# Kernel tuning notes

Measured on AMD Instinct MI355X. Metric: run time of the kernel, lower is better.

## Reference

```python
import jax, jax.numpy as jnp
import numpy as np

N_HEADS = 16
ROPE_BASE = 10000.0


def _rotate_half(x):
    d = x.shape[-1] // 2
    return jnp.concatenate([-x[..., d:], x[..., :d]], axis=-1)


def _rope_tables(L, head_dim, dtype):
    inv_freq = 1.0 / (ROPE_BASE ** (jnp.arange(0, head_dim, 2, dtype=jnp.float32) / head_dim))
    t = jnp.arange(L, dtype=jnp.float32)
    freqs = jnp.outer(t, inv_freq)  # [L, head_dim//2]
    # torch code repeats cos/sin along last dim (tile x2) -> concat([c, c])
    cos = jnp.concatenate([jnp.cos(freqs), jnp.cos(freqs)], axis=-1).astype(dtype)
    sin = jnp.concatenate([jnp.sin(freqs), jnp.sin(freqs)], axis=-1).astype(dtype)
    return cos[None, None], sin[None, None]  # [1,1,L,head_dim]


def setup_inputs() -> dict:
    key = jax.random.key(0)
    kx, kq, kk, kv, ko = jax.random.split(key, 5)
    B, L, D = 4, 2048, 1024
    s = 0.02
    return {
        "x": jax.random.normal(kx, (B, L, D), dtype=jnp.float32),
        "Wq": jax.random.normal(kq, (D, D), dtype=jnp.float32) * s,
        "Wk": jax.random.normal(kk, (D, D), dtype=jnp.float32) * s,
        "Wv": jax.random.normal(kv, (D, D), dtype=jnp.float32) * s,
        "Wo": jax.random.normal(ko, (D, D), dtype=jnp.float32) * s,
    }


def reference(x, Wq, Wk, Wv, Wo):
    B, L, D = x.shape
    H = N_HEADS
    hd = D // H

    def split_heads(y):
        return y.reshape(B, L, H, hd).transpose(0, 2, 1, 3)  # [B,H,L,hd]

    q = split_heads(x @ Wq.T)
    k = split_heads(x @ Wk.T)
    v = split_heads(x @ Wv.T)

    cos, sin = _rope_tables(L, hd, x.dtype)
    q = q * cos + _rotate_half(q) * sin
    k = k * cos + _rotate_half(k) * sin

    scale = 1.0 / jnp.sqrt(jnp.asarray(hd, dtype=x.dtype))
    scores = jnp.einsum("bhqd,bhkd->bhqk", q, k) * scale
    attn = jax.nn.softmax(scores, axis=-1)
    out = jnp.einsum("bhqk,bhkd->bhqd", attn, v)
    out = out.transpose(0, 2, 1, 3).reshape(B, L, D)
    return out @ Wo.T
```

## Files before the change

### kernel.cpp

```cpp
#include <hip/hip_runtime.h>


typedef __bf16 bf16_t;
typedef __bf16 bf16x8 __attribute__((ext_vector_type(8)));
typedef __bf16 bf16x4 __attribute__((ext_vector_type(4)));
typedef float  floatx4 __attribute__((ext_vector_type(4)));
typedef unsigned int u32x2 __attribute__((ext_vector_type(2)));

#define B_  4
#define L_  2048
#define D_  1024
#define H_  16
#define HD_ 64
#define M_  (B_*L_)

__device__ __forceinline__ void async_copy16(const bf16_t* g, bf16_t* l) {
  __builtin_amdgcn_global_load_lds(
      (const __attribute__((address_space(1))) void*)g,
      (__attribute__((address_space(3))) void*)l, 16, 0, 0);
}

__device__ __forceinline__ unsigned int pack_bf16(float a, float b) {
  unsigned short ua = __builtin_bit_cast(unsigned short, (bf16_t)a);
  unsigned short ub = __builtin_bit_cast(unsigned short, (bf16_t)b);
  return (unsigned int)ua | ((unsigned int)ub << 16);
}

__device__ __forceinline__ unsigned int cvt_pk(float lo, float hi) {
  unsigned int r;
  asm("v_cvt_pk_bf16_f32 %0, %1, %2" : "=v"(r) : "v"(lo), "v"(hi));
  return r;
}

__global__ void prep_kernel(const float* __restrict__ x,
                            const float* __restrict__ wq, const float* __restrict__ wk,
                            const float* __restrict__ wv, const float* __restrict__ wo,
                            bf16_t* __restrict__ xb,
                            bf16_t* __restrict__ wqb, bf16_t* __restrict__ wkb,
                            bf16_t* __restrict__ wvb, bf16_t* __restrict__ wob,
                            float* __restrict__ cosT, float* __restrict__ sinT)
{
  const int NX = M_*D_;
  const int NW = D_*D_;
  int i = blockIdx.x*256 + threadIdx.x;
  if (i < NX) { xb[i] = (bf16_t)x[i]; return; }
  i -= NX;
  if (i < NW) { wqb[i] = (bf16_t)wq[i]; return; }
  i -= NW;
  if (i < NW) { wkb[i] = (bf16_t)wk[i]; return; }
  i -= NW;
  if (i < NW) { wvb[i] = (bf16_t)wv[i]; return; }
  i -= NW;
  if (i < NW) { wob[i] = (bf16_t)wo[i]; return; }
  i -= NW;
  if (i < L_*32) {
    int f = i >> 11, l = i & 2047;
    double inv = pow(10000.0, -(double)f / 32.0);
    double ang = (double)l * inv;
    cosT[i] = (float)cos(ang);
    sinT[i] = (float)sin(ang);
  }
}

template<int MODE>
__global__ __launch_bounds__(256) void gemm_kernel(
    const bf16_t* __restrict__ A,
    const bf16_t* __restrict__ W0, const bf16_t* __restrict__ W1, const bf16_t* __restrict__ W2,
    bf16_t* __restrict__ C0, bf16_t* __restrict__ C1, bf16_t* __restrict__ C2,
    float* __restrict__ Cf,
    const float* __restrict__ cosT, const float* __restrict__ sinT)
{
  __shared__ __align__(16) bf16_t Sh[16384];
  bf16_t* As = Sh;
  bf16_t* Bs = Sh + 8192;
  const int KD = 1024, ND = 1024;
  int z = (MODE==0) ? (int)blockIdx.z : 0;
  const bf16_t* W = (MODE==1) ? W0 : (z==0 ? W0 : (z==1 ? W1 : W2));
  int m0 = blockIdx.x*128, n0 = blockIdx.y*128;
  int tid = threadIdx.x;
  int wave = tid>>6, lane = tid&63, quad = lane>>4, lr = lane&15;
  int wm = wave>>1, wn = wave&1;
  int srow = lane>>3, sslot = lane&7;

  floatx4 zero4 = {0.f,0.f,0.f,0.f};
  floatx4 acc[4][4];
  #pragma unroll
  for (int i=0;i<4;i++)
    #pragma unroll
    for (int j=0;j<4;j++) acc[i][j] = zero4;

  #pragma unroll 1
  for (int k0 = 0; k0 < KD; k0 += 64) {
    #pragma unroll
    for (int j=0;j<4;j++) {
      int chunk = wave + j*4;
      int row = chunk*8 + srow;
      int col = ((sslot ^ (row&7)) << 3);
      async_copy16(A + (size_t)(m0+row)*KD + k0 + col, &As[chunk*512]);
      async_copy16(W + (size_t)(n0+row)*KD + k0 + col, &Bs[chunk*512]);
    }
    __syncthreads();
    #pragma unroll
    for (int ks=0; ks<2; ks++) {
      bf16x8 af[4], bfr[4];
      #pragma unroll
      for (int mi=0;mi<4;mi++)
        af[mi] = *(const bf16x8*)&As[(wm*64+mi*16+lr)*64 + (((ks*4+quad) ^ (lr&7))<<3)];
      #pragma unroll
      for (int ni=0;ni<4;ni++)
        bfr[ni] = *(const bf16x8*)&Bs[(wn*64+ni*16+lr)*64 + (((ks*4+quad) ^ (lr&7))<<3)];
      #pragma unroll
      for (int mi=0;mi<4;mi++)
        #pragma unroll
        for (int ni=0;ni<4;ni++)
          acc[mi][ni] = __builtin_amdgcn_mfma_f32_16x16x32_bf16(af[mi], bfr[ni], acc[mi][ni], 0,0,0);
    }
    __syncthreads();
  }

  if (MODE==1) {
    #pragma unroll
    for (int mi=0;mi<4;mi++) {
      int row = m0 + wm*64 + mi*16 + quad*4;
      #pragma unroll
      for (int ni=0;ni<4;ni++) {
        int col = n0 + wn*64 + ni*16 + lr;
        #pragma unroll
        for (int r=0;r<4;r++)
          Cf[(size_t)(row+r)*ND + col] = acc[mi][ni][r];
      }
    }
  } else if (z < 2) {
    bf16_t* Cb = (z==0) ? C0 : C1;
    const float sc = (z==0) ? 0.18033688011112042f : 1.0f;
    #pragma unroll
    for (int mi=0;mi<4;mi++) {
      int row = m0 + wm*64 + mi*16 + quad*4;
      int l = row & 2047;
      #pragma unroll
      for (int ni=0;ni<2;ni++) {
        int col = n0 + wn*64 + ni*16 + lr;
        int f = ni*16 + lr;
        float4 cv = *(const float4*)&cosT[f*2048 + l];
        float4 sv = *(const float4*)&sinT[f*2048 + l];
        #pragma unroll
        for (int r=0;r<4;r++) {
          float c = (&cv.x)[r];
          float s = (&sv.x)[r];
          float lo = acc[mi][ni][r], hi = acc[mi][ni+2][r];
          Cb[(size_t)(row+r)*ND + col]      = (bf16_t)((lo*c - hi*s)*sc);
          Cb[(size_t)(row+r)*ND + col + 32] = (bf16_t)((hi*c + lo*s)*sc);
        }
      }
    }
  } else {
    #pragma unroll
    for (int mi=0;mi<4;mi++) {
      int rowm = wm*64 + mi*16 + quad*4;
      #pragma unroll
      for (int ni=0;ni<4;ni++) {
        int coln = wn*64 + ni*16 + lr;
        uint2 val;
        val.x = pack_bf16(acc[mi][ni][0], acc[mi][ni][1]);
        val.y = pack_bf16(acc[mi][ni][2], acc[mi][ni][3]);
        *(uint2*)&Sh[coln*128 + (rowm ^ ((coln&15)<<3))] = val;
      }
    }
    __syncthreads();
    int bb = m0 >> 11, l0 = m0 & 2047;
    #pragma unroll
    for (int rep=0; rep<8; rep++) {
      int idx = rep*256 + tid;
      int coln = idx >> 4, seg = idx & 15;
      bf16x8 v = *(const bf16x8*)&Sh[coln*128 + ((seg*8) ^ ((coln&15)<<3))];
      int cg = n0 + coln;
      *(bf16x8*)&C2[((size_t)((bb<<4) + (cg>>6))*64 + (cg&63))*2048 + l0 + seg*8] = v;
    }
  }
}

__global__ __launch_bounds__(256) void attn_kernel(
    const bf16_t* __restrict__ Q, const bf16_t* __restrict__ K,
    const bf16_t* __restrict__ Vt, bf16_t* __restrict__ O)
{
  __shared__ __align__(16) bf16_t Ks[3][4096];
  __shared__ __align__(16) bf16_t Vs[3][4096];
  int tid = threadIdx.x;
  int wave = tid>>6, lane = tid&63, quad = lane>>4, lr = lane&15;
  int bh = blockIdx.x; int b = bh>>4, h = bh&15;
  int q0 = blockIdx.y*128 + wave*32;
  size_t rowQ = (size_t)b*L_ + q0;

  int slr = (lr&3) | ((lr&4)<<1) | ((lr&8)>>1);
  int srow8 = lane>>3;
  int sslot = lane&7;

  bf16x8 qf[2][2];
  #pragma unroll
  for (int n=0;n<2;n++)
    #pragma unroll
    for (int ks=0;ks<2;ks++)
      qf[n][ks] = *(const bf16x8*)&Q[(rowQ + n*16 + lr)*D_ + h*HD_ + ks*32 + quad*8];

  const bf16_t* Kg = K + (size_t)b*L_*D_ + h*HD_;
  const bf16_t* Vg = Vt + (size_t)bh*HD_*L_;

  bf16x8 onesf;
  #pragma unroll
  for (int j=0;j<8;j++) onesf[j] = (bf16_t)1.0f;

  floatx4 zero4 = {0.f,0.f,0.f,0.f};
  floatx4 accO[2][4];
  floatx4 accS[2];
  accS[0] = zero4; accS[1] = zero4;
  #pragma unroll
  for (int n=0;n<2;n++)
    #pragma unroll
    for (int dt=0;dt<4;dt++) accO[n][dt] = zero4;

  auto stage = [&](int it, int c) {
    #pragma unroll
    for (int j=0;j<2;j++) {
      int row = wave*16 + j*8 + srow8;
      int col = ((sslot ^ (row&7)) << 3);
      async_copy16(Kg + (size_t)(it*64 + row)*D_ + col, &Ks[c][(wave*16 + j*8)*64]);
      async_copy16(Vg + (size_t)row*L_ + it*64 + col,   &Vs[c][(wave*16 + j*8)*64]);
    }
  };

  stage(0, 0);
  stage(1, 1);
  asm volatile("s_waitcnt vmcnt(4)" ::: "memory");
  __builtin_amdgcn_s_barrier();

#define ATTN_BODY(IT, CC, DO_STAGE)                                           \
  {                                                                           \
    if (DO_STAGE) stage((IT)+2, ((CC)+2)%3);                                  \
    floatx4 St[2][4];                                                         \
    _Pragma("unroll")                                                         \
    for (int t=0;t<4;t++) { St[0][t]=zero4; St[1][t]=zero4; }                 \
    _Pragma("unroll")                                                         \
    for (int t=0;t<4;t++) {                                                   \
      _Pragma("unroll")                                                       \
      for (int ks=0;ks<2;ks++) {                                              \
        bf16x8 kf = *(const bf16x8*)&Ks[CC][(t*16+slr)*64 + (((ks*4+quad) ^ (slr&7))<<3)]; \
        St[0][t] = __builtin_amdgcn_mfma_f32_16x16x32_bf16(kf, qf[0][ks], St[0][t], 0,0,0); \
        St[1][t] = __builtin_amdgcn_mfma_f32_16x16x32_bf16(kf, qf[1][ks], St[1][t], 0,0,0); \
      }                                                                       \
    }                                                                         \
    bf16x8 pfv[2][2];                                                         \
    _Pragma("unroll")                                                         \
    for (int n=0;n<2;n++) {                                                   \
      _Pragma("unroll")                                                       \
      for (int hh=0;hh<2;hh++) {                                              \
        unsigned int w00 = cvt_pk(exp2f(St[n][2*hh][0]),   exp2f(St[n][2*hh][1]));   \
        unsigned int w01 = cvt_pk(exp2f(St[n][2*hh][2]),   exp2f(St[n][2*hh][3]));   \
        unsigned int w10 = cvt_pk(exp2f(St[n][2*hh+1][0]), exp2f(St[n][2*hh+1][1])); \
        unsigned int w11 = cvt_pk(exp2f(St[n][2*hh+1][2]), exp2f(St[n][2*hh+1][3])); \
        u32x2 r0 = __builtin_amdgcn_permlane32_swap(w00, w10, false, false);  \
        u32x2 r1 = __builtin_amdgcn_permlane32_swap(w01, w11, false, false);  \
        union { unsigned int u[4]; bf16x8 v; } pu;                            \
        pu.u[0] = r0.x; pu.u[1] = r1.x; pu.u[2] = r0.y; pu.u[3] = r1.y;       \
        pfv[n][hh] = pu.v;                                                    \
      }                                                                       \
    }                                                                         \
    _Pragma("unroll")                                                         \
    for (int dt=0;dt<4;dt++) {                                                \
      _Pragma("unroll")                                                       \
      for (int hh=0;hh<2;hh++) {                                              \
        bf16x8 vf = *(const bf16x8*)&Vs[CC][(dt*16+lr)*64 + (((hh*4+quad) ^ (lr&7))<<3)]; \
        accO[0][dt] = __builtin_amdgcn_mfma_f32_16x16x32_bf16(vf, pfv[0][hh], accO[0][dt], 0,0,0); \
        accO[1][dt] = __builtin_amdgcn_mfma_f32_16x16x32_bf16(vf, pfv[1][hh], accO[1][dt], 0,0,0); \
      }                                                                       \
    }                                                                         \
    accS[0] = __builtin_amdgcn_mfma_f32_16x16x32_bf16(onesf, pfv[0][0], accS[0], 0,0,0); \
    accS[1] = __builtin_amdgcn_mfma_f32_16x16x32_bf16(onesf, pfv[1][0], accS[1], 0,0,0); \
    accS[0] = __builtin_amdgcn_mfma_f32_16x16x32_bf16(onesf, pfv[0][1], accS[0], 0,0,0); \
    accS[1] = __builtin_amdgcn_mfma_f32_16x16x32_bf16(onesf, pfv[1][1], accS[1], 0,0,0); \
    if (DO_STAGE) { asm volatile("s_waitcnt vmcnt(4)" ::: "memory"); }        \
    else          { asm volatile("s_waitcnt vmcnt(0)" ::: "memory"); }        \
    __builtin_amdgcn_s_barrier();                                             \
  }

  #pragma unroll 1
  for (int itb = 0; itb < 30; itb += 3) {
    ATTN_BODY(itb+0, 0, true);
    ATTN_BODY(itb+1, 1, true);
    ATTN_BODY(itb+2, 2, true);
  }
  ATTN_BODY(30, 0, false);
  ATTN_BODY(31, 1, false);
#undef ATTN_BODY

  float inv0 = 1.0f / accS[0][0];
  float inv1 = 1.0f / accS[1][0];
  #pragma unroll
  for (int n=0;n<2;n++) {
    float inv = n ? inv1 : inv0;
    #pragma unroll
    for (int dt=0;dt<4;dt++) {
      uint2 w;
      w.x = cvt_pk(accO[n][dt][0]*inv, accO[n][dt][1]*inv);
      w.y = cvt_pk(accO[n][dt][2]*inv, accO[n][dt][3]*inv);
      *(uint2*)&O[(rowQ + n*16 + lr)*D_ + h*HD_ + dt*16 + quad*4] = w;
    }
  }
}

extern "C" void kernel_launch(void* const* d_in, const int* in_sizes, int n_in,
                              void* d_out, int out_size, void* d_ws, size_t ws_size,
                              hipStream_t stream) {
  const float* x  = (const float*)d_in[0];
  const float* wq = (const float*)d_in[1];
  const float* wk = (const float*)d_in[2];
  const float* wv = (const float*)d_in[3];
  const float* wo = (const float*)d_in[4];

  char* ws = (char*)d_ws;
  bf16_t* xb  = (bf16_t*)(ws);
  bf16_t* Qb  = (bf16_t*)(ws + (size_t)(16u<<20));
  bf16_t* Kb  = (bf16_t*)(ws + (size_t)(32u<<20));
  bf16_t* Vtb = (bf16_t*)(ws + (size_t)(48u<<20));
  bf16_t* wqb = (bf16_t*)(ws + (size_t)(64u<<20));
  bf16_t* wkb = (bf16_t*)(ws + (size_t)(66u<<20));
  bf16_t* wvb = (bf16_t*)(ws + (size_t)(68u<<20));
  bf16_t* wob = (bf16_t*)(ws + (size_t)(70u<<20));
  float* cosT = (float*)(ws + (size_t)(72u<<20));
  float* sinT = (float*)(ws + (size_t)(72u<<20) + (256u<<10));
  bf16_t* Ob = xb;

  prep_kernel<<<49408, 256, 0, stream>>>(x, wq, wk, wv, wo, xb, wqb, wkb, wvb, wob, cosT, sinT);
  gemm_kernel<0><<<dim3(64,8,3), 256, 0, stream>>>(xb, wqb, wkb, wvb, Qb, Kb, Vtb, nullptr, cosT, sinT);
  attn_kernel<<<dim3(64,16), 256, 0, stream>>>(Qb, Kb, Vtb, Ob);
  gemm_kernel<1><<<dim3(64,8,1), 256, 0, stream>>>(Ob, wob, nullptr, nullptr,
                                                   nullptr, nullptr, nullptr, (float*)d_out, cosT, sinT);
}
```

Measured before the change: 302.8 us.

## Vectorize fp32-to-bf16 prep and software-pipeline QK^T one tile ahead in attention

The prep kernel now converts eight floats per thread using float4 loads and a bf16x8 store, which cuts the grid size and the number of memory instructions. The attention loop now double-buffers the score accumulators. It computes the next tile's QK^T MFMAs between the current tile's exp/pack step and its PV MFMAs, so softmax ALU work can overlap matrix work. The wait before each barrier becomes vmcnt(0), which may expose more load latency. The extra score registers raise register pressure and could reduce occupancy.

```diff
diff --git a/kernel.cpp b/kernel.cpp
--- a/kernel.cpp
+++ b/kernel.cpp
@@ -40,19 +40,28 @@
                             bf16_t* __restrict__ wvb, bf16_t* __restrict__ wob,
                             float* __restrict__ cosT, float* __restrict__ sinT)
 {
-  const int NX = M_*D_;
-  const int NW = D_*D_;
+  const int NXv = (M_*D_) >> 3;
+  const int NWv = (D_*D_) >> 3;
+  const int NC  = NXv + 4*NWv;
   int i = blockIdx.x*256 + threadIdx.x;
-  if (i < NX) { xb[i] = (bf16_t)x[i]; return; }
-  i -= NX;
-  if (i < NW) { wqb[i] = (bf16_t)wq[i]; return; }
-  i -= NW;
-  if (i < NW) { wkb[i] = (bf16_t)wk[i]; return; }
-  i -= NW;
-  if (i < NW) { wvb[i] = (bf16_t)wv[i]; return; }
-  i -= NW;
-  if (i < NW) { wob[i] = (bf16_t)wo[i]; return; }
-  i -= NW;
+  if (i < NC) {
+    const float* s; bf16_t* d; size_t o;
+    if (i < NXv) { s = x; d = xb; o = (size_t)i << 3; }
+    else {
+      int r = i - NXv; int w = r >> 17;
+      o = (size_t)(r & (NWv-1)) << 3;
+      s = (w==0)?wq:(w==1)?wk:(w==2)?wv:wo;
+      d = (w==0)?wqb:(w==1)?wkb:(w==2)?wvb:wob;
+    }
+    float4 a = *(const float4*)(s+o);
+    float4 b = *(const float4*)(s+o+4);
+    bf16x8 v;
+    v[0]=(bf16_t)a.x; v[1]=(bf16_t)a.y; v[2]=(bf16_t)a.z; v[3]=(bf16_t)a.w;
+    v[4]=(bf16_t)b.x; v[5]=(bf16_t)b.y; v[6]=(bf16_t)b.z; v[7]=(bf16_t)b.w;
+    *(bf16x8*)(d+o) = v;
+    return;
+  }
+  i -= NC;
   if (i < L_*32) {
     int f = i >> 11, l = i & 2047;
     double inv = pow(10000.0, -(double)f / 32.0);
@@ -218,6 +227,8 @@
     #pragma unroll
     for (int dt=0;dt<4;dt++) accO[n][dt] = zero4;
 
+  floatx4 StA[2][4], StB[2][4];
+
   auto stage = [&](int it, int c) {
     #pragma unroll
     for (int j=0;j<2;j++) {
@@ -230,33 +241,36 @@
 
   stage(0, 0);
   stage(1, 1);
-  asm volatile("s_waitcnt vmcnt(4)" ::: "memory");
+  asm volatile("s_waitcnt vmcnt(0)" ::: "memory");
   __builtin_amdgcn_s_barrier();
 
-#define ATTN_BODY(IT, CC, DO_STAGE)                                           \
-  {                                                                           \
-    if (DO_STAGE) stage((IT)+2, ((CC)+2)%3);                                  \
-    floatx4 St[2][4];                                                         \
+#define QKT_M(CN, SN)                                                         \
     _Pragma("unroll")                                                         \
-    for (int t=0;t<4;t++) { St[0][t]=zero4; St[1][t]=zero4; }                 \
+    for (int t=0;t<4;t++) { SN[0][t]=zero4; SN[1][t]=zero4; }                 \
     _Pragma("unroll")                                                         \
     for (int t=0;t<4;t++) {                                                   \
       _Pragma("unroll")                                                       \
       for (int ks=0;ks<2;ks++) {                                              \
-        bf16x8 kf = *(const bf16x8*)&Ks[CC][(t*16+slr)*64 + (((ks*4+quad) ^ (slr&7))<<3)]; \
-        St[0][t] = __builtin_amdgcn_mfma_f32_16x16x32_bf16(kf, qf[0][ks], St[0][t], 0,0,0); \
-        St[1][t] = __builtin_amdgcn_mfma_f32_16x16x32_bf16(kf, qf[1][ks], St[1][t], 0,0,0); \
+        bf16x8 kf = *(const bf16x8*)&Ks[CN][(t*16+slr)*64 + (((ks*4+quad) ^ (slr&7))<<3)]; \
+        SN[0][t] = __builtin_amdgcn_mfma_f32_16x16x32_bf16(kf, qf[0][ks], SN[0][t], 0,0,0); \
+        SN[1][t] = __builtin_amdgcn_mfma_f32_16x16x32_bf16(kf, qf[1][ks], SN[1][t], 0,0,0); \
       }                                                                       \
-    }                                                                         \
+    }
+
+  QKT_M(0, StA)
+
+#define ATTN_BODY(IT, CC, SC, SN, DO_STAGE, DO_QKT, DO_SYNC)                  \
+  {                                                                           \
+    if (DO_STAGE) stage((IT)+2, ((CC)+2)%3);                                  \
     bf16x8 pfv[2][2];                                                         \
     _Pragma("unroll")                                                         \
     for (int n=0;n<2;n++) {                                                   \
       _Pragma("unroll")                                                       \
       for (int hh=0;hh<2;hh++) {                                              \
-        unsigned int w00 = cvt_pk(exp2f(St[n][2*hh][0]),   exp2f(St[n][2*hh][1]));   \
-        unsigned int w01 = cvt_pk(exp2f(St[n][2*hh][2]),   exp2f(St[n][2*hh][3]));   \
-        unsigned int w10 = cvt_pk(exp2f(St[n][2*hh+1][0]), exp2f(St[n][2*hh+1][1])); \
-        unsigned int w11 = cvt_pk(exp2f(St[n][2*hh+1][2]), exp2f(St[n][2*hh+1][3])); \
+        unsigned int w00 = cvt_pk(exp2f(SC[n][2*hh][0]),   exp2f(SC[n][2*hh][1]));   \
+        unsigned int w01 = cvt_pk(exp2f(SC[n][2*hh][2]),   exp2f(SC[n][2*hh][3]));   \
+        unsigned int w10 = cvt_pk(exp2f(SC[n][2*hh+1][0]), exp2f(SC[n][2*hh+1][1])); \
+        unsigned int w11 = cvt_pk(exp2f(SC[n][2*hh+1][2]), exp2f(SC[n][2*hh+1][3])); \
         u32x2 r0 = __builtin_amdgcn_permlane32_swap(w00, w10, false, false);  \
         u32x2 r1 = __builtin_amdgcn_permlane32_swap(w01, w11, false, false);  \
         union { unsigned int u[4]; bf16x8 v; } pu;                            \
@@ -264,6 +278,7 @@
         pfv[n][hh] = pu.v;                                                    \
       }                                                                       \
     }                                                                         \
+    if (DO_QKT) { QKT_M(((CC)+1)%3, SN) }                                     \
     _Pragma("unroll")                                                         \
     for (int dt=0;dt<4;dt++) {                                                \
       _Pragma("unroll")                                                       \
@@ -277,20 +292,25 @@
     accS[1] = __builtin_amdgcn_mfma_f32_16x16x32_bf16(onesf, pfv[1][0], accS[1], 0,0,0); \
     accS[0] = __builtin_amdgcn_mfma_f32_16x16x32_bf16(onesf, pfv[0][1], accS[0], 0,0,0); \
     accS[1] = __builtin_amdgcn_mfma_f32_16x16x32_bf16(onesf, pfv[1][1], accS[1], 0,0,0); \
-    if (DO_STAGE) { asm volatile("s_waitcnt vmcnt(4)" ::: "memory"); }        \
-    else          { asm volatile("s_waitcnt vmcnt(0)" ::: "memory"); }        \
-    __builtin_amdgcn_s_barrier();                                             \
+    if (DO_SYNC) {                                                            \
+      asm volatile("s_waitcnt vmcnt(0)" ::: "memory");                        \
+      __builtin_amdgcn_s_barrier();                                           \
+    }                                                                         \
   }
 
   #pragma unroll 1
-  for (int itb = 0; itb < 30; itb += 3) {
-    ATTN_BODY(itb+0, 0, true);
-    ATTN_BODY(itb+1, 1, true);
-    ATTN_BODY(itb+2, 2, true);
-  }
-  ATTN_BODY(30, 0, false);
-  ATTN_BODY(31, 1, false);
+  for (int itb = 0; itb < 30; itb += 6) {
+    ATTN_BODY(itb+0, 0, StA, StB, true, true, true);
+    ATTN_BODY(itb+1, 1, StB, StA, true, true, true);
+    ATTN_BODY(itb+2, 2, StA, StB, true, true, true);
+    ATTN_BODY(itb+3, 0, StB, StA, true, true, true);
+    ATTN_BODY(itb+4, 1, StA, StB, true, true, true);
+    ATTN_BODY(itb+5, 2, StB, StA, true, true, true);
+  }
+  ATTN_BODY(30, 0, StA, StB, false, true,  false);
+  ATTN_BODY(31, 1, StB, StA, false, false, false);
 #undef ATTN_BODY
+#undef QKT_M
 
   float inv0 = 1.0f / accS[0][0];
   float inv1 = 1.0f / accS[1][0];
@@ -329,7 +349,7 @@
   float* sinT = (float*)(ws + (size_t)(72u<<20) + (256u<<10));
   bf16_t* Ob = xb;
 
-  prep_kernel<<<49408, 256, 0, stream>>>(x, wq, wk, wv, wo, xb, wqb, wkb, wvb, wob, cosT, sinT);
+  prep_kernel<<<6400, 256, 0, stream>>>(x, wq, wk, wv, wo, xb, wqb, wkb, wvb, wob, cosT, sinT);
   gemm_kernel<0><<<dim3(64,8,3), 256, 0, stream>>>(xb, wqb, wkb, wvb, Qb, Kb, Vtb, nullptr, cosT, sinT);
   attn_kernel<<<dim3(64,16), 256, 0, stream>>>(Qb, Kb, Vtb, Ob);
   gemm_kernel<1><<<dim3(64,8,1), 256, 0, stream>>>(Ob, wob, nullptr, nullptr,
```

Result: faster. 288.9 us (-4.6%).
